# Optimization experiments

Hardware: AMD Instinct MI355X
Metric: run time of the kernel (lower is better)

Reference implementation:

```python
import jax, jax.numpy as jnp
import numpy as np

B, T, TA = 16, 512, 1024
D_REG, D_AUD, HID, HEADS = 512, 512, 256, 4
NREG = 4  # mouth, left_eye, right_eye, nose (dict order)
N = NREG * B * T + B * TA  # total graph nodes


def _build_edges():
    # Faithful, vectorized version of build_graph's edge construction (phoneme_times=None).
    bs = np.arange(B)[:, None]
    ts = np.arange(T)[None, :]
    src, dst = [], []
    # cross-region same-timestep edges, all ordered pairs i != j (edge_attr 0)
    for i in range(NREG):
        for j in range(NREG):
            if i != j:
                n1 = i * B * T + bs * T + ts
                n2 = j * B * T + bs * T + ts
                src.append(n1.ravel()); dst.append(n2.ravel())
    # temporal edges within each region (edge_attr 1)
    tt = np.arange(T - 1)[None, :]
    for i in range(NREG):
        n1 = i * B * T + bs * T + tt
        src.append(n1.ravel()); dst.append((n1 + 1).ravel())
    # eye (region idx 1,2) -> audio alignment edges (edge_attr 3)
    t_aud = (np.arange(T)[None, :] * TA) // T
    audio_start = NREG * B * T
    for i in (1, 2):
        n_eye = i * B * T + bs * T + ts
        n_aud = audio_start + bs * TA + t_aud
        src.append(n_eye.ravel()); dst.append(np.broadcast_to(n_aud, (B, T)).ravel())
    # self loops (PyG GATConv default add_self_loops=True)
    loops = np.arange(N)
    src.append(loops); dst.append(loops)
    return np.concatenate(src).astype(np.int32), np.concatenate(dst).astype(np.int32)


def setup_inputs() -> dict:
    key = jax.random.key(0)
    ks = iter(jax.random.split(key, 48))
    def rn(shape, scale=1.0):
        return jax.random.normal(next(ks), shape, dtype=jnp.float32) * jnp.float32(scale)
    src_np, dst_np = _build_edges()
    inp = {
        'mouth': rn((B, T, D_REG)), 'left_eye': rn((B, T, D_REG)),
        'right_eye': rn((B, T, D_REG)), 'nose': rn((B, T, D_REG)),
        'audio_embeddings': rn((B, TA, D_AUD)),
    }
    s = 1.0 / np.sqrt(D_REG)
    for name in ['mouth', 'left_eye', 'right_eye', 'nose']:
        inp['w_' + name] = rn((D_REG, HID), s)
        inp['b_' + name] = jnp.zeros((HID,), jnp.float32)
    inp['w_audio'] = rn((D_AUD, HID), 1.0 / np.sqrt(D_AUD))
    inp['b_audio'] = jnp.zeros((HID,), jnp.float32)
    # GAT layers: layer 0 in=HID, layers 1,2 in=HID*HEADS; layers 0,1 concat, layer 2 averages heads
    dims_in = [HID, HID * HEADS, HID * HEADS]
    for l, din in enumerate(dims_in):
        concat = l < 2
        inp[f'W{l}'] = rn((din, HEADS * HID), 1.0 / np.sqrt(din))
        inp[f'as{l}'] = rn((HEADS, HID), 0.1)
        inp[f'ad{l}'] = rn((HEADS, HID), 0.1)
        inp[f'bias{l}'] = jnp.zeros((HEADS * HID,) if concat else (HID,), jnp.float32)
    inp['ln_g'] = jnp.ones((HID,), jnp.float32)
    inp['ln_b'] = jnp.zeros((HID,), jnp.float32)
    inp['src'] = jnp.asarray(src_np)
    inp['dst'] = jnp.asarray(dst_np)
    return inp


def _gat(x, W, a_s, a_d, bias, src, dst, concat):
    # PyG GATConv (eval mode): gather -> per-head attention softmax over dst -> scatter-add
    H, C = a_s.shape
    h = (x @ W).reshape(-1, H, C)                      # [N,H,C]
    alpha_s = jnp.sum(h * a_s, -1)                     # [N,H]
    alpha_d = jnp.sum(h * a_d, -1)                     # [N,H]
    e = jax.nn.leaky_relu(alpha_s[src] + alpha_d[dst], 0.2)  # [E,H]
    m = jax.ops.segment_max(e, dst, num_segments=N)
    ex = jnp.exp(e - m[dst])
    denom = jax.ops.segment_sum(ex, dst, num_segments=N)
    alpha = ex / (denom[dst] + jnp.float32(1e-16))
    out = jax.ops.segment_sum(h[src] * alpha[:, :, None], dst, num_segments=N)  # [N,H,C]
    out = out.reshape(-1, H * C) if concat else out.mean(1)
    return out + bias


def _forward(mouth, left_eye, right_eye, nose, audio_embeddings,
             w_mouth, b_mouth, w_left_eye, b_left_eye, w_right_eye, b_right_eye,
             w_nose, b_nose, w_audio, b_audio,
             W0, as0, ad0, bias0, W1, as1, ad1, bias1, W2, as2, ad2, bias2,
             ln_g, ln_b, src, dst):
    x = jnp.concatenate([
        (mouth @ w_mouth + b_mouth).reshape(B * T, HID),
        (left_eye @ w_left_eye + b_left_eye).reshape(B * T, HID),
        (right_eye @ w_right_eye + b_right_eye).reshape(B * T, HID),
        (nose @ w_nose + b_nose).reshape(B * T, HID),
        (audio_embeddings @ w_audio + b_audio).reshape(B * TA, HID),
    ], axis=0)                                          # [N,HID]
    x = _gat(x, W0, as0, ad0, bias0, src, dst, True)    # [N,HID*HEADS]
    x = _gat(x, W1, as1, ad1, bias1, src, dst, True)    # [N,HID*HEADS]
    x = _gat(x, W2, as2, ad2, bias2, src, dst, False)   # [N,HID]
    mu = x.mean(-1, keepdims=True)
    var = jnp.mean(jnp.square(x - mu), -1, keepdims=True)
    x = (x - mu) / jnp.sqrt(var + jnp.float32(1e-5)) * ln_g + ln_b
    nodes_pb = NREG * T + TA
    return x.reshape(B, nodes_pb, HID).mean(1)          # [B,HID]


def reference(mouth, left_eye, right_eye, nose, audio_embeddings,
              w_mouth, b_mouth, w_left_eye, b_left_eye, w_right_eye, b_right_eye,
              w_nose, b_nose, w_audio, b_audio,
              W0, as0, ad0, bias0, W1, as1, ad1, bias1, W2, as2, ad2, bias2,
              ln_g, ln_b, src, dst):
    return _forward(mouth, left_eye, right_eye, nose, audio_embeddings,
                    w_mouth, b_mouth, w_left_eye, b_left_eye, w_right_eye, b_right_eye,
                    w_nose, b_nose, w_audio, b_audio,
                    W0, as0, ad0, bias0, W1, as1, ad1, bias1, W2, as2, ad2, bias2,
                    ln_g, ln_b, src, dst)
```

## Files before the change

kernel.cpp:

```cpp
#include <hip/hip_runtime.h>


typedef unsigned short u16;
typedef unsigned int u32;
typedef __bf16 bf16x8 __attribute__((ext_vector_type(8)));
typedef float f32x4 __attribute__((ext_vector_type(4)));

#define ASYNC16(gp, lp)                                                        \
  __builtin_amdgcn_global_load_lds(                                            \
      (const __attribute__((address_space(1))) void*)(gp),                     \
      (__attribute__((address_space(3))) void*)(lp), 16, 0, 0)

__device__ __forceinline__ u16 f2bf(float f) {
  union { float f; u32 u; } v; v.f = f;
  u32 u = v.u + 0x7FFFu + ((v.u >> 16) & 1u);
  return (u16)(u >> 16);
}
__device__ __forceinline__ float bf2f(u16 x) {
  union { u32 u; float f; } v; v.u = ((u32)x) << 16;
  return v.f;
}
__device__ __forceinline__ float4 load_bf4(const u16* p) {
  ushort4 s = *(const ushort4*)p;
  float4 r; r.x = bf2f(s.x); r.y = bf2f(s.y); r.z = bf2f(s.z); r.w = bf2f(s.w);
  return r;
}
__device__ __forceinline__ float lrelu(float v) { return v > 0.f ? v : 0.2f * v; }
__device__ __forceinline__ float dot4(float4 a, float4 b) {
  return a.x * b.x + a.y * b.y + a.z * b.z + a.w * b.w;
}
__device__ __forceinline__ float wred(float v) {
#pragma unroll
  for (int off = 32; off; off >>= 1) v += __shfl_down(v, off);
  return v;
}
__device__ __forceinline__ float wredx(float v) {
#pragma unroll
  for (int off = 32; off; off >>= 1) v += __shfl_xor(v, off);
  return v;
}

struct PK { const float* W[8]; u16* P[8]; int KB[8]; int NN[8]; int st[9]; };
__global__ __launch_bounds__(256) void pack_kernel(PK p) {
  const int f = blockIdx.x * 4 + (threadIdx.x >> 6);
  const int lane = threadIdx.x & 63;
  int e = 0;
  while (f >= p.st[e + 1]) ++e;
  const int local = f - p.st[e];
  const int KB = p.KB[e], N = p.NN[e];
  const int nt = local / KB, kb = local % KB;
  const float* W = p.W[e] + (size_t)(kb * 32 + (lane >> 4) * 8) * N + nt * 16 + (lane & 15);
  u16* dst = p.P[e] + ((size_t)local * 64 + lane) * 8;
  u16 o[8];
#pragma unroll
  for (int j = 0; j < 8; ++j) o[j] = f2bf(W[(size_t)j * N]);
  *(uint4*)dst = *(uint4*)o;
}

__global__ __launch_bounds__(256) void gemm_kernel(
    const u16* __restrict__ A, const u16* __restrict__ Bp, u16* __restrict__ C,
    int K, int ldc) {
  __shared__ __align__(16) u16 As[2][2][128 * 32];
  const int KB = K >> 5;
  const int KB2 = K >> 6;
  const int w = blockIdx.y * 8 + blockIdx.x;
  const int xcd = w & 7, m = w >> 3;
  const int blockCol = (m & 7) * 128;
  const int blockRow = ((m >> 3) * 8 + xcd) * 128;
  const int tid = threadIdx.x;
  const int wave = tid >> 6, lane = tid & 63;
  const int wr = (wave >> 1) * 64, wc = (wave & 1) * 64;
  const int lr = lane & 15, lq = lane >> 4;
  const int sRow = wave * 16 + (lane >> 2);
  const int sGc = (lane & 3) ^ ((sRow >> 1) & 3);
  const size_t aOff0 = (size_t)(blockRow + sRow) * K + sGc * 8;
  const size_t aOff1 = aOff0 + (size_t)64 * K;
  const int ldsOff0 = wave * 512;
  const int ldsOff1 = 2048 + wave * 512;

  const u16* Bn[4];
#pragma unroll
  for (int ni = 0; ni < 4; ++ni)
    Bn[ni] = Bp + ((size_t)(((blockCol + wc) >> 4) + ni) * KB) * 512 + lane * 8;

  f32x4 acc[4][4] = {};

#pragma unroll
  for (int h = 0; h < 2; ++h) {
    ASYNC16(A + aOff0 + h * 32, As[0][h] + ldsOff0);
    ASYNC16(A + aOff1 + h * 32, As[0][h] + ldsOff1);
  }
  __syncthreads();

  for (int kb2 = 0; kb2 < KB2; ++kb2) {
    const int cb = kb2 & 1;
    if (kb2 + 1 < KB2) {
      const size_t k1 = (size_t)(kb2 + 1) * 64;
#pragma unroll
      for (int h = 0; h < 2; ++h) {
        ASYNC16(A + aOff0 + k1 + h * 32, As[cb ^ 1][h] + ldsOff0);
        ASYNC16(A + aOff1 + k1 + h * 32, As[cb ^ 1][h] + ldsOff1);
      }
    }
#pragma unroll
    for (int h = 0; h < 2; ++h) {
      const int kb = kb2 * 2 + h;
      const u16* cur = As[cb][h];
      bf16x8 bfr[4];
#pragma unroll
      for (int ni = 0; ni < 4; ++ni)
        bfr[ni] = *(const bf16x8*)(Bn[ni] + (size_t)kb * 512);
      bf16x8 af[4];
#pragma unroll
      for (int mi = 0; mi < 4; ++mi) {
        const int R = wr + mi * 16 + lr;
        const int cp = lq ^ ((R >> 1) & 3);
        af[mi] = *(const bf16x8*)(cur + R * 32 + cp * 8);
      }
#pragma unroll
      for (int mi = 0; mi < 4; ++mi)
#pragma unroll
        for (int ni = 0; ni < 4; ++ni)
          acc[mi][ni] = __builtin_amdgcn_mfma_f32_16x16x32_bf16(af[mi], bfr[ni],
                                                                acc[mi][ni], 0, 0, 0);
    }
    __syncthreads();
  }
#pragma unroll
  for (int mi = 0; mi < 4; ++mi)
#pragma unroll
    for (int ni = 0; ni < 4; ++ni) {
      const int col = blockCol + wc + ni * 16 + lr;
#pragma unroll
      for (int r = 0; r < 4; ++r) {
        const int row = blockRow + wr + mi * 16 + lq * 4 + r;
        C[(size_t)row * ldc + col] = f2bf(acc[mi][ni][r]);
      }
    }
}

struct ProjArgs { const float* x[5]; const u16* w[5]; const float* b[5]; };
__global__ __launch_bounds__(256) void proj_kernel(ProjArgs pa,
                                                   u16* __restrict__ C) {
  __shared__ __align__(16) u16 As[128 * 32];
  const int blockRow = blockIdx.y * 128, blockCol = blockIdx.x * 128;
  const int reg = blockRow >= 32768 ? 4 : (blockRow >> 13);
  const int regBase = reg == 4 ? 32768 : reg * 8192;
  const float* Af = pa.x[reg] + (size_t)(blockRow - regBase) * 512;
  const u16* Bp = pa.w[reg];
  const int tid = threadIdx.x;
  const int wave = tid >> 6, lane = tid & 63;
  const int wr = (wave >> 1) * 64, wc = (wave & 1) * 64;
  const int lr = lane & 15, lq = lane >> 4;
  const int rr = tid >> 2;
  const int cphys = tid & 3;
  const int sGc = cphys ^ ((tid >> 3) & 3);

  const u16* Bn[4];
#pragma unroll
  for (int ni = 0; ni < 4; ++ni)
    Bn[ni] = Bp + ((size_t)(((blockCol + wc) >> 4) + ni) * 16) * 512 + lane * 8;

  f32x4 acc[4][4] = {};

  for (int k0 = 0; k0 < 512; k0 += 32) {
    __syncthreads();
    bf16x8 bfr[4];
#pragma unroll
    for (int ni = 0; ni < 4; ++ni)
      bfr[ni] = *(const bf16x8*)(Bn[ni] + (size_t)k0 * 16);
#pragma unroll
    for (int i = 0; i < 2; ++i) {
      const int row = i * 64 + rr;
      const float* ap = Af + (size_t)row * 512 + k0 + sGc * 8;
      float4 f0 = *(const float4*)(ap);
      float4 f1 = *(const float4*)(ap + 4);
      uint4 pk;
      pk.x = (u32)f2bf(f0.x) | ((u32)f2bf(f0.y) << 16);
      pk.y = (u32)f2bf(f0.z) | ((u32)f2bf(f0.w) << 16);
      pk.z = (u32)f2bf(f1.x) | ((u32)f2bf(f1.y) << 16);
      pk.w = (u32)f2bf(f1.z) | ((u32)f2bf(f1.w) << 16);
      *(uint4*)(&As[row * 32 + cphys * 8]) = pk;
    }
    __syncthreads();
    bf16x8 af[4];
#pragma unroll
    for (int mi = 0; mi < 4; ++mi) {
      const int R = wr + mi * 16 + lr;
      const int cp = lq ^ ((R >> 1) & 3);
      af[mi] = *(const bf16x8*)(&As[R * 32 + cp * 8]);
    }
#pragma unroll
    for (int mi = 0; mi < 4; ++mi)
#pragma unroll
      for (int ni = 0; ni < 4; ++ni)
        acc[mi][ni] = __builtin_amdgcn_mfma_f32_16x16x32_bf16(af[mi], bfr[ni],
                                                              acc[mi][ni], 0, 0, 0);
  }
  const float* bias = pa.b[reg];
#pragma unroll
  for (int mi = 0; mi < 4; ++mi)
#pragma unroll
    for (int ni = 0; ni < 4; ++ni) {
      const int col = blockCol + wc + ni * 16 + lr;
      const float bv = bias[col];
#pragma unroll
      for (int r = 0; r < 4; ++r) {
        const int row = blockRow + wr + mi * 16 + lq * 4 + r;
        C[(size_t)row * 256 + col] = f2bf(acc[mi][ni][r] + bv);
      }
    }
}

template <bool MEAN>
__global__ __launch_bounds__(256) void agg_kernel(
    const u16* __restrict__ h, const float* __restrict__ a_s,
    const float* __restrict__ a_d, const float* __restrict__ bias,
    void* __restrict__ out) {
  extern __shared__ float red[];
  const int tid = threadIdx.x;
  const int head = tid >> 6, lane = tid & 63;
  const int c4 = tid * 4;
  const float4 sa = *(const float4*)(a_s + c4);
  const float4 da = *(const float4*)(a_d + c4);
  __shared__ float asL[4][4], adL[4][4], apL[4][4], aeS[4], aeD[4];
  __shared__ float alpha[4][4][5], alphaA[4][3];

  const int bt = blockIdx.x;
  const int b = bt >> 9, t = bt & 511;
  const bool hasPrev = t > 0;
  const int nodeE = 32768 + b * 1024 + 2 * t;
  const int nodeO = nodeE + 1;

  float4 hv[4], hp[4];
#pragma unroll
  for (int r = 0; r < 4; ++r)
    hv[r] = load_bf4(h + (size_t)(r * 8192 + bt) * 1024 + c4);
  float4 hae = load_bf4(h + (size_t)nodeE * 1024 + c4);
  float4 hao = load_bf4(h + (size_t)nodeO * 1024 + c4);
  if (hasPrev) {
#pragma unroll
    for (int r = 0; r < 4; ++r)
      hp[r] = load_bf4(h + (size_t)(r * 8192 + bt - 1) * 1024 + c4);
  }
#pragma unroll
  for (int r = 0; r < 4; ++r) {
    float ss = wred(dot4(hv[r], sa));
    float dd = wred(dot4(hv[r], da));
    float sp = hasPrev ? wred(dot4(hp[r], sa)) : 0.f;
    if (lane == 0) { asL[r][head] = ss; adL[r][head] = dd; apL[r][head] = sp; }
  }
  {
    float se = wred(dot4(hae, sa));
    float de = wred(dot4(hae, da));
    if (lane == 0) { aeS[head] = se; aeD[head] = de; }
  }
  __syncthreads();
  if (tid < 16) {
    const int j = tid >> 2, hh = tid & 3;
    const float ad = adL[j][hh];
    float e[5];
#pragma unroll
    for (int r = 0; r < 4; ++r) e[r] = lrelu(asL[r][hh] + ad);
    int cnt = 4;
    if (hasPrev) { e[4] = lrelu(apL[j][hh] + ad); cnt = 5; }
    float mx = e[0];
    for (int k = 1; k < cnt; ++k) mx = fmaxf(mx, e[k]);
    float s = 0.f, ex[5];
    for (int k = 0; k < cnt; ++k) { ex[k] = __expf(e[k] - mx); s += ex[k]; }
    const float inv = 1.f / (s + 1e-16f);
#pragma unroll
    for (int k = 0; k < 5; ++k) alpha[j][hh][k] = (k < cnt) ? ex[k] * inv : 0.f;
  } else if (tid < 20) {
    const int hh = tid - 16;
    const float ad = aeD[hh];
    const float e0 = lrelu(aeS[hh] + ad);
    const float e1 = lrelu(asL[1][hh] + ad);
    const float e2 = lrelu(asL[2][hh] + ad);
    const float mx = fmaxf(e0, fmaxf(e1, e2));
    const float x0 = __expf(e0 - mx), x1 = __expf(e1 - mx), x2 = __expf(e2 - mx);
    const float inv = 1.f / (x0 + x1 + x2 + 1e-16f);
    alphaA[hh][0] = x0 * inv; alphaA[hh][1] = x1 * inv; alphaA[hh][2] = x2 * inv;
  }
  __syncthreads();

  float4 av[6];
#pragma unroll
  for (int j = 0; j < 4; ++j) {
    const float* al = &alpha[j][head][0];
    float4 acc;
    acc.x = al[0] * hv[0].x + al[1] * hv[1].x + al[2] * hv[2].x + al[3] * hv[3].x;
    acc.y = al[0] * hv[0].y + al[1] * hv[1].y + al[2] * hv[2].y + al[3] * hv[3].y;
    acc.z = al[0] * hv[0].z + al[1] * hv[1].z + al[2] * hv[2].z + al[3] * hv[3].z;
    acc.w = al[0] * hv[0].w + al[1] * hv[1].w + al[2] * hv[2].w + al[3] * hv[3].w;
    if (hasPrev) {
      const float a4 = al[4];
      acc.x += a4 * hp[j].x; acc.y += a4 * hp[j].y;
      acc.z += a4 * hp[j].z; acc.w += a4 * hp[j].w;
    }
    av[j] = acc;
  }
  {
    const float a0 = alphaA[head][0], a1 = alphaA[head][1], a2 = alphaA[head][2];
    float4 acc;
    acc.x = a0 * hae.x + a1 * hv[1].x + a2 * hv[2].x;
    acc.y = a0 * hae.y + a1 * hv[1].y + a2 * hv[2].y;
    acc.z = a0 * hae.z + a1 * hv[1].z + a2 * hv[2].z;
    acc.w = a0 * hae.w + a1 * hv[1].w + a2 * hv[2].w;
    av[4] = acc;
    av[5] = hao;
  }

  if constexpr (!MEAN) {
    const float4 bv = *(const float4*)(bias + c4);
    u16* ob = (u16*)out;
    size_t rows[6];
#pragma unroll
    for (int j = 0; j < 4; ++j) rows[j] = (size_t)(j * 8192 + bt);
    rows[4] = (size_t)nodeE; rows[5] = (size_t)nodeO;
#pragma unroll
    for (int k = 0; k < 6; ++k) {
      ushort4 o;
      o.x = f2bf(av[k].x + bv.x); o.y = f2bf(av[k].y + bv.y);
      o.z = f2bf(av[k].z + bv.z); o.w = f2bf(av[k].w + bv.w);
      *(ushort4*)(ob + rows[k] * 1024 + c4) = o;
    }
  } else {
#pragma unroll
    for (int k = 0; k < 6; ++k) *(float4*)(&red[k * 1024 + c4]) = av[k];
    __syncthreads();
    const float bb = bias[tid];
    float* of = (float*)out;
    size_t rows[6];
#pragma unroll
    for (int j = 0; j < 4; ++j) rows[j] = (size_t)(j * 8192 + bt);
    rows[4] = (size_t)nodeE; rows[5] = (size_t)nodeO;
#pragma unroll
    for (int k = 0; k < 6; ++k) {
      const float v = 0.25f * (red[k * 1024 + tid] + red[k * 1024 + tid + 256] +
                               red[k * 1024 + tid + 512] + red[k * 1024 + tid + 768]) + bb;
      of[rows[k] * 256 + tid] = v;
    }
  }
}

__global__ __launch_bounds__(256) void ln_pool_kernel(
    const float* __restrict__ xf, const float* __restrict__ g,
    const float* __restrict__ bb, float* __restrict__ part) {
  const int tid = threadIdx.x;
  const int wave = tid >> 6, lane = tid & 63;
  const int node0 = blockIdx.x * 64 + wave * 16;
  const float4 g4 = *(const float4*)(g + lane * 4);
  const float4 b4 = *(const float4*)(bb + lane * 4);
  float4 acc = {0.f, 0.f, 0.f, 0.f};
  for (int i = 0; i < 16; ++i) {
    const float4 v = *(const float4*)(xf + (size_t)(node0 + i) * 256 + lane * 4);
    const float s = wredx(v.x + v.y + v.z + v.w);
    const float q = wredx(v.x * v.x + v.y * v.y + v.z * v.z + v.w * v.w);
    const float mean = s * (1.f / 256.f);
    const float var = q * (1.f / 256.f) - mean * mean;
    const float rstd = rsqrtf(var + 1e-5f);
    acc.x += (v.x - mean) * rstd * g4.x + b4.x;
    acc.y += (v.y - mean) * rstd * g4.y + b4.y;
    acc.z += (v.z - mean) * rstd * g4.z + b4.z;
    acc.w += (v.w - mean) * rstd * g4.w + b4.w;
  }
  *(float4*)(part + (size_t)(blockIdx.x * 4 + wave) * 256 + lane * 4) = acc;
}

__global__ __launch_bounds__(256) void pool2_kernel(const float* __restrict__ part,
                                                    float* __restrict__ out) {
  const int chunk = blockIdx.x;
  const int c = threadIdx.x;
  float s = 0.f;
  for (int i = 0; i < 192; ++i) s += part[(size_t)(chunk * 192 + i) * 256 + c];
  out[chunk * 256 + c] = s * (1.f / 3072.f);
}

extern "C" void kernel_launch(void* const* d_in, const int* in_sizes, int n_in,
                              void* d_out, int out_size, void* d_ws, size_t ws_size,
                              hipStream_t stream) {
  const float* x_reg[4] = {(const float*)d_in[0], (const float*)d_in[1],
                           (const float*)d_in[2], (const float*)d_in[3]};
  const float* audio = (const float*)d_in[4];
  const float* w_reg[4] = {(const float*)d_in[5], (const float*)d_in[7],
                           (const float*)d_in[9], (const float*)d_in[11]};
  const float* b_reg[4] = {(const float*)d_in[6], (const float*)d_in[8],
                           (const float*)d_in[10], (const float*)d_in[12]};
  const float* w_aud = (const float*)d_in[13];
  const float* b_aud = (const float*)d_in[14];
  const float* Wl[3] = {(const float*)d_in[15], (const float*)d_in[19],
                        (const float*)d_in[23]};
  const float* as_in[3] = {(const float*)d_in[16], (const float*)d_in[20],
                           (const float*)d_in[24]};
  const float* ad_in[3] = {(const float*)d_in[17], (const float*)d_in[21],
                           (const float*)d_in[25]};
  const float* bias_l[3] = {(const float*)d_in[18], (const float*)d_in[22],
                            (const float*)d_in[26]};
  const float* ln_g = (const float*)d_in[27];
  const float* ln_b = (const float*)d_in[28];

  char* ws = (char*)d_ws;
  u16* h_bf = (u16*)ws;
  float* part = (float*)ws;
  u16* xb = (u16*)(ws + 100663296);
  float* xf = (float*)xb;
  u16* wt = (u16*)(ws + 201326592);

  u16* wtp[5];
  for (int r = 0; r < 5; ++r) wtp[r] = wt + (size_t)r * 131072;
  u16* wt0 = wt + 655360;
  u16* wt1 = wt + 917504;
  u16* wt2 = wt + 1966080;

  PK pk;
  for (int r = 0; r < 4; ++r) { pk.W[r] = w_reg[r]; pk.P[r] = wtp[r]; pk.KB[r] = 16; pk.NN[r] = 256; }
  pk.W[4] = w_aud; pk.P[4] = wtp[4]; pk.KB[4] = 16; pk.NN[4] = 256;
  pk.W[5] = Wl[0]; pk.P[5] = wt0; pk.KB[5] = 8;  pk.NN[5] = 1024;
  pk.W[6] = Wl[1]; pk.P[6] = wt1; pk.KB[6] = 32; pk.NN[6] = 1024;
  pk.W[7] = Wl[2]; pk.P[7] = wt2; pk.KB[7] = 32; pk.NN[7] = 1024;
  pk.st[0] = 0;
  {
    const int nfr[8] = {256, 256, 256, 256, 256, 512, 2048, 2048};
    int acc = 0;
    for (int e = 0; e < 8; ++e) { acc += nfr[e]; pk.st[e + 1] = acc; }
  }
  pack_kernel<<<pk.st[8] / 4, 256, 0, stream>>>(pk);

  ProjArgs pa;
  for (int r = 0; r < 4; ++r) { pa.x[r] = x_reg[r]; pa.w[r] = wtp[r]; pa.b[r] = b_reg[r]; }
  pa.x[4] = audio; pa.w[4] = wtp[4]; pa.b[4] = b_aud;
  proj_kernel<<<dim3(2, 384), 256, 0, stream>>>(pa, xb);

  const u16* wl[3] = {wt0, wt1, wt2};
  const int Kl[3] = {256, 1024, 1024};
  const size_t dynLds = 6 * 1024 * sizeof(float);
  for (int l = 0; l < 3; ++l) {
    gemm_kernel<<<dim3(8, 384), 256, 0, stream>>>(xb, wl[l], h_bf, Kl[l], 1024);
    if (l < 2)
      agg_kernel<false><<<8192, 256, 0, stream>>>(h_bf, as_in[l], ad_in[l],
                                                  bias_l[l], xb);
    else
      agg_kernel<true><<<8192, 256, dynLds, stream>>>(h_bf, as_in[l], ad_in[l],
                                                      bias_l[l], xf);
  }

  ln_pool_kernel<<<768, 256, 0, stream>>>(xf, ln_g, ln_b, part);
  pool2_kernel<<<16, 256, 0, stream>>>(part, (float*)d_out);
}
```

Before: 616.9 us.

## Fold input projection into GAT layer-0 weights and drop agg shared-memory syncs

Precomputes combined weights W_region·W0 and biases b_region·W0 on device, so one K=512 GEMM per region writes layer-0 features directly. This removes the separate projection GEMM and its intermediate write/read. The layer-0/1 aggregation now computes attention with xor-shuffle reductions in every lane instead of LDS plus two barriers. The GEMM also hoists both B-fragment loads ahead of the async A prefetch. Folding the weights raises the layer-0 GEMM from K=256 to K=512 and adds several small setup kernels plus an extra bf16 rounding of the combined weights.

Result: slower. 690.7 us (+12.0%).

```diff
diff --git a/kernel.cpp b/kernel.cpp
--- a/kernel.cpp
+++ b/kernel.cpp
@@ -40,7 +40,7 @@
   return v;
 }
 
-struct PK { const float* W[8]; u16* P[8]; int KB[8]; int NN[8]; int st[9]; };
+struct PK { const float* W[3]; u16* P[3]; int KB[3]; int NN[3]; int st[4]; };
 __global__ __launch_bounds__(256) void pack_kernel(PK p) {
   const int f = blockIdx.x * 4 + (threadIdx.x >> 6);
   const int lane = threadIdx.x & 63;
@@ -55,6 +55,41 @@
 #pragma unroll
   for (int j = 0; j < 8; ++j) o[j] = f2bf(W[(size_t)j * N]);
   *(uint4*)dst = *(uint4*)o;
+}
+
+struct CW { const float* w[5]; };
+__global__ __launch_bounds__(256) void cvtw_kernel(CW a, u16* __restrict__ dst) {
+  const int i = blockIdx.x * 256 + threadIdx.x;
+  const float* src = a.w[i >> 15];
+  float4 v = ((const float4*)src)[i & 32767];
+  ushort4 o;
+  o.x = f2bf(v.x); o.y = f2bf(v.y); o.z = f2bf(v.z); o.w = f2bf(v.w);
+  ((ushort4*)dst)[i] = o;
+}
+
+struct BC { const float* br[5]; };
+__global__ __launch_bounds__(256) void bc_kernel(BC a, const float* __restrict__ W0,
+                                                 float* __restrict__ bc) {
+  const int r = blockIdx.x >> 2;
+  const int n = (blockIdx.x & 3) * 256 + threadIdx.x;
+  const float* b = a.br[r];
+  float acc = 0.f;
+  for (int k = 0; k < 256; ++k) acc += b[k] * W0[(size_t)k * 1024 + n];
+  bc[r * 1024 + n] = acc;
+}
+
+__global__ __launch_bounds__(256) void packwc_kernel(const u16* __restrict__ Wrm,
+                                                     u16* __restrict__ P) {
+  const int f = blockIdx.x * 4 + (threadIdx.x >> 6);
+  const int lane = threadIdx.x & 63;
+  const int region = f >> 10, local = f & 1023;
+  const int nt = local >> 4, kb = local & 15;
+  const u16* W = Wrm + (size_t)(region * 512 + kb * 32 + (lane >> 4) * 8) * 1024 +
+                 nt * 16 + (lane & 15);
+  u16 o[8];
+#pragma unroll
+  for (int j = 0; j < 8; ++j) o[j] = W[(size_t)j * 1024];
+  *(uint4*)(P + ((size_t)f * 64 + lane) * 8) = *(uint4*)o;
 }
 
 __global__ __launch_bounds__(256) void gemm_kernel(
@@ -94,6 +129,12 @@
 
   for (int kb2 = 0; kb2 < KB2; ++kb2) {
     const int cb = kb2 & 1;
+    bf16x8 bfr[2][4];
+#pragma unroll
+    for (int h = 0; h < 2; ++h)
+#pragma unroll
+      for (int ni = 0; ni < 4; ++ni)
+        bfr[h][ni] = *(const bf16x8*)(Bn[ni] + (size_t)(kb2 * 2 + h) * 512);
     if (kb2 + 1 < KB2) {
       const size_t k1 = (size_t)(kb2 + 1) * 64;
 #pragma unroll
@@ -104,12 +145,7 @@
     }
 #pragma unroll
     for (int h = 0; h < 2; ++h) {
-      const int kb = kb2 * 2 + h;
       const u16* cur = As[cb][h];
-      bf16x8 bfr[4];
-#pragma unroll
-      for (int ni = 0; ni < 4; ++ni)
-        bfr[ni] = *(const bf16x8*)(Bn[ni] + (size_t)kb * 512);
       bf16x8 af[4];
 #pragma unroll
       for (int mi = 0; mi < 4; ++mi) {
@@ -121,7 +157,7 @@
       for (int mi = 0; mi < 4; ++mi)
 #pragma unroll
         for (int ni = 0; ni < 4; ++ni)
-          acc[mi][ni] = __builtin_amdgcn_mfma_f32_16x16x32_bf16(af[mi], bfr[ni],
+          acc[mi][ni] = __builtin_amdgcn_mfma_f32_16x16x32_bf16(af[mi], bfr[h][ni],
                                                                 acc[mi][ni], 0, 0, 0);
     }
     __syncthreads();
@@ -139,15 +175,20 @@
     }
 }
 
-struct ProjArgs { const float* x[5]; const u16* w[5]; const float* b[5]; };
-__global__ __launch_bounds__(256) void proj_kernel(ProjArgs pa,
-                                                   u16* __restrict__ C) {
+struct P0Args { const float* x[5]; };
+__global__ __launch_bounds__(256) void projL0_kernel(P0Args pa,
+                                                     const u16* __restrict__ Bp0,
+                                                     const float* __restrict__ bc,
+                                                     u16* __restrict__ C) {
   __shared__ __align__(16) u16 As[128 * 32];
-  const int blockRow = blockIdx.y * 128, blockCol = blockIdx.x * 128;
+  const int w = blockIdx.y * 8 + blockIdx.x;
+  const int xcd = w & 7, m = w >> 3;
+  const int blockCol = (m & 7) * 128;
+  const int blockRow = ((m >> 3) * 8 + xcd) * 128;
   const int reg = blockRow >= 32768 ? 4 : (blockRow >> 13);
   const int regBase = reg == 4 ? 32768 : reg * 8192;
   const float* Af = pa.x[reg] + (size_t)(blockRow - regBase) * 512;
-  const u16* Bp = pa.w[reg];
+  const u16* Bp = Bp0 + (size_t)reg * 524288;
   const int tid = threadIdx.x;
   const int wave = tid >> 6, lane = tid & 63;
   const int wr = (wave >> 1) * 64, wc = (wave & 1) * 64;
@@ -197,7 +238,7 @@
         acc[mi][ni] = __builtin_amdgcn_mfma_f32_16x16x32_bf16(af[mi], bfr[ni],
                                                               acc[mi][ni], 0, 0, 0);
   }
-  const float* bias = pa.b[reg];
+  const float* bias = bc + reg * 1024;
 #pragma unroll
   for (int mi = 0; mi < 4; ++mi)
 #pragma unroll
@@ -207,7 +248,7 @@
 #pragma unroll
       for (int r = 0; r < 4; ++r) {
         const int row = blockRow + wr + mi * 16 + lq * 4 + r;
-        C[(size_t)row * 256 + col] = f2bf(acc[mi][ni][r] + bv);
+        C[(size_t)row * 1024 + col] = f2bf(acc[mi][ni][r] + bv);
       }
     }
 }
@@ -223,8 +264,6 @@
   const int c4 = tid * 4;
   const float4 sa = *(const float4*)(a_s + c4);
   const float4 da = *(const float4*)(a_d + c4);
-  __shared__ float asL[4][4], adL[4][4], apL[4][4], aeS[4], aeD[4];
-  __shared__ float alpha[4][4][5], alphaA[4][3];
 
   const int bt = blockIdx.x;
   const int b = bt >> 9, t = bt & 511;
@@ -243,89 +282,142 @@
     for (int r = 0; r < 4; ++r)
       hp[r] = load_bf4(h + (size_t)(r * 8192 + bt - 1) * 1024 + c4);
   }
-#pragma unroll
-  for (int r = 0; r < 4; ++r) {
-    float ss = wred(dot4(hv[r], sa));
-    float dd = wred(dot4(hv[r], da));
-    float sp = hasPrev ? wred(dot4(hp[r], sa)) : 0.f;
-    if (lane == 0) { asL[r][head] = ss; adL[r][head] = dd; apL[r][head] = sp; }
-  }
-  {
-    float se = wred(dot4(hae, sa));
-    float de = wred(dot4(hae, da));
-    if (lane == 0) { aeS[head] = se; aeD[head] = de; }
-  }
-  __syncthreads();
-  if (tid < 16) {
-    const int j = tid >> 2, hh = tid & 3;
-    const float ad = adL[j][hh];
-    float e[5];
-#pragma unroll
-    for (int r = 0; r < 4; ++r) e[r] = lrelu(asL[r][hh] + ad);
-    int cnt = 4;
-    if (hasPrev) { e[4] = lrelu(apL[j][hh] + ad); cnt = 5; }
-    float mx = e[0];
-    for (int k = 1; k < cnt; ++k) mx = fmaxf(mx, e[k]);
-    float s = 0.f, ex[5];
-    for (int k = 0; k < cnt; ++k) { ex[k] = __expf(e[k] - mx); s += ex[k]; }
-    const float inv = 1.f / (s + 1e-16f);
-#pragma unroll
-    for (int k = 0; k < 5; ++k) alpha[j][hh][k] = (k < cnt) ? ex[k] * inv : 0.f;
-  } else if (tid < 20) {
-    const int hh = tid - 16;
-    const float ad = aeD[hh];
-    const float e0 = lrelu(aeS[hh] + ad);
-    const float e1 = lrelu(asL[1][hh] + ad);
-    const float e2 = lrelu(asL[2][hh] + ad);
-    const float mx = fmaxf(e0, fmaxf(e1, e2));
-    const float x0 = __expf(e0 - mx), x1 = __expf(e1 - mx), x2 = __expf(e2 - mx);
-    const float inv = 1.f / (x0 + x1 + x2 + 1e-16f);
-    alphaA[hh][0] = x0 * inv; alphaA[hh][1] = x1 * inv; alphaA[hh][2] = x2 * inv;
-  }
-  __syncthreads();
-
-  float4 av[6];
-#pragma unroll
-  for (int j = 0; j < 4; ++j) {
-    const float* al = &alpha[j][head][0];
-    float4 acc;
-    acc.x = al[0] * hv[0].x + al[1] * hv[1].x + al[2] * hv[2].x + al[3] * hv[3].x;
-    acc.y = al[0] * hv[0].y + al[1] * hv[1].y + al[2] * hv[2].y + al[3] * hv[3].y;
-    acc.z = al[0] * hv[0].z + al[1] * hv[1].z + al[2] * hv[2].z + al[3] * hv[3].z;
-    acc.w = al[0] * hv[0].w + al[1] * hv[1].w + al[2] * hv[2].w + al[3] * hv[3].w;
+
+  if constexpr (!MEAN) {
+    float ss[4], dd[4], sp[4];
+#pragma unroll
+    for (int r = 0; r < 4; ++r) {
+      ss[r] = wredx(dot4(hv[r], sa));
+      dd[r] = wredx(dot4(hv[r], da));
+    }
     if (hasPrev) {
-      const float a4 = al[4];
-      acc.x += a4 * hp[j].x; acc.y += a4 * hp[j].y;
-      acc.z += a4 * hp[j].z; acc.w += a4 * hp[j].w;
-    }
-    av[j] = acc;
-  }
-  {
-    const float a0 = alphaA[head][0], a1 = alphaA[head][1], a2 = alphaA[head][2];
-    float4 acc;
-    acc.x = a0 * hae.x + a1 * hv[1].x + a2 * hv[2].x;
-    acc.y = a0 * hae.y + a1 * hv[1].y + a2 * hv[2].y;
-    acc.z = a0 * hae.z + a1 * hv[1].z + a2 * hv[2].z;
-    acc.w = a0 * hae.w + a1 * hv[1].w + a2 * hv[2].w;
-    av[4] = acc;
-    av[5] = hao;
-  }
-
-  if constexpr (!MEAN) {
+#pragma unroll
+      for (int r = 0; r < 4; ++r) sp[r] = wredx(dot4(hp[r], sa));
+    }
+    const float se = wredx(dot4(hae, sa));
+    const float de = wredx(dot4(hae, da));
+
     const float4 bv = *(const float4*)(bias + c4);
     u16* ob = (u16*)out;
-    size_t rows[6];
-#pragma unroll
-    for (int j = 0; j < 4; ++j) rows[j] = (size_t)(j * 8192 + bt);
-    rows[4] = (size_t)nodeE; rows[5] = (size_t)nodeO;
-#pragma unroll
-    for (int k = 0; k < 6; ++k) {
+#pragma unroll
+    for (int j = 0; j < 4; ++j) {
+      const float ad = dd[j];
+      float e0 = lrelu(ss[0] + ad), e1 = lrelu(ss[1] + ad);
+      float e2 = lrelu(ss[2] + ad), e3 = lrelu(ss[3] + ad);
+      float mx = fmaxf(fmaxf(e0, e1), fmaxf(e2, e3));
+      float e4 = 0.f;
+      if (hasPrev) { e4 = lrelu(sp[j] + ad); mx = fmaxf(mx, e4); }
+      const float x0 = __expf(e0 - mx), x1 = __expf(e1 - mx);
+      const float x2 = __expf(e2 - mx), x3 = __expf(e3 - mx);
+      const float x4 = hasPrev ? __expf(e4 - mx) : 0.f;
+      const float inv = 1.f / (x0 + x1 + x2 + x3 + x4 + 1e-16f);
+      const float a0 = x0 * inv, a1 = x1 * inv, a2 = x2 * inv, a3 = x3 * inv;
+      const float a4 = x4 * inv;
+      float4 acc;
+      acc.x = a0 * hv[0].x + a1 * hv[1].x + a2 * hv[2].x + a3 * hv[3].x;
+      acc.y = a0 * hv[0].y + a1 * hv[1].y + a2 * hv[2].y + a3 * hv[3].y;
+      acc.z = a0 * hv[0].z + a1 * hv[1].z + a2 * hv[2].z + a3 * hv[3].z;
+      acc.w = a0 * hv[0].w + a1 * hv[1].w + a2 * hv[2].w + a3 * hv[3].w;
+      if (hasPrev) {
+        acc.x += a4 * hp[j].x; acc.y += a4 * hp[j].y;
+        acc.z += a4 * hp[j].z; acc.w += a4 * hp[j].w;
+      }
       ushort4 o;
-      o.x = f2bf(av[k].x + bv.x); o.y = f2bf(av[k].y + bv.y);
-      o.z = f2bf(av[k].z + bv.z); o.w = f2bf(av[k].w + bv.w);
-      *(ushort4*)(ob + rows[k] * 1024 + c4) = o;
+      o.x = f2bf(acc.x + bv.x); o.y = f2bf(acc.y + bv.y);
+      o.z = f2bf(acc.z + bv.z); o.w = f2bf(acc.w + bv.w);
+      *(ushort4*)(ob + (size_t)(j * 8192 + bt) * 1024 + c4) = o;
+    }
+    {
+      const float e0 = lrelu(se + de);
+      const float e1 = lrelu(ss[1] + de);
+      const float e2 = lrelu(ss[2] + de);
+      const float mx = fmaxf(e0, fmaxf(e1, e2));
+      const float x0 = __expf(e0 - mx), x1 = __expf(e1 - mx), x2 = __expf(e2 - mx);
+      const float inv = 1.f / (x0 + x1 + x2 + 1e-16f);
+      const float a0 = x0 * inv, a1 = x1 * inv, a2 = x2 * inv;
+      float4 acc;
+      acc.x = a0 * hae.x + a1 * hv[1].x + a2 * hv[2].x;
+      acc.y = a0 * hae.y + a1 * hv[1].y + a2 * hv[2].y;
+      acc.z = a0 * hae.z + a1 * hv[1].z + a2 * hv[2].z;
+      acc.w = a0 * hae.w + a1 * hv[1].w + a2 * hv[2].w;
+      ushort4 oe, oo;
+      oe.x = f2bf(acc.x + bv.x); oe.y = f2bf(acc.y + bv.y);
+      oe.z = f2bf(acc.z + bv.z); oe.w = f2bf(acc.w + bv.w);
+      oo.x = f2bf(hao.x + bv.x); oo.y = f2bf(hao.y + bv.y);
+      oo.z = f2bf(hao.z + bv.z); oo.w = f2bf(hao.w + bv.w);
+      *(ushort4*)(ob + (size_t)nodeE * 1024 + c4) = oe;
+      *(ushort4*)(ob + (size_t)nodeO * 1024 + c4) = oo;
     }
   } else {
+    __shared__ float asL[4][4], adL[4][4], apL[4][4], aeS[4], aeD[4];
+    __shared__ float alpha[4][4][5], alphaA[4][3];
+#pragma unroll
+    for (int r = 0; r < 4; ++r) {
+      float ss = wred(dot4(hv[r], sa));
+      float dd = wred(dot4(hv[r], da));
+      float sp = hasPrev ? wred(dot4(hp[r], sa)) : 0.f;
+      if (lane == 0) { asL[r][head] = ss; adL[r][head] = dd; apL[r][head] = sp; }
+    }
+    {
+      float sev = wred(dot4(hae, sa));
+      float dev = wred(dot4(hae, da));
+      if (lane == 0) { aeS[head] = sev; aeD[head] = dev; }
+    }
+    __syncthreads();
+    if (tid < 16) {
+      const int j = tid >> 2, hh = tid & 3;
+      const float ad = adL[j][hh];
+      float e[5];
+#pragma unroll
+      for (int r = 0; r < 4; ++r) e[r] = lrelu(asL[r][hh] + ad);
+      int cnt = 4;
+      if (hasPrev) { e[4] = lrelu(apL[j][hh] + ad); cnt = 5; }
+      float mx = e[0];
+      for (int k = 1; k < cnt; ++k) mx = fmaxf(mx, e[k]);
+      float s = 0.f, ex[5];
+      for (int k = 0; k < cnt; ++k) { ex[k] = __expf(e[k] - mx); s += ex[k]; }
+      const float inv = 1.f / (s + 1e-16f);
+#pragma unroll
+      for (int k = 0; k < 5; ++k) alpha[j][hh][k] = (k < cnt) ? ex[k] * inv : 0.f;
+    } else if (tid < 20) {
+      const int hh = tid - 16;
+      const float ad = aeD[hh];
+      const float e0 = lrelu(aeS[hh] + ad);
+      const float e1 = lrelu(asL[1][hh] + ad);
+      const float e2 = lrelu(asL[2][hh] + ad);
+      const float mx = fmaxf(e0, fmaxf(e1, e2));
+      const float x0 = __expf(e0 - mx), x1 = __expf(e1 - mx), x2 = __expf(e2 - mx);
+      const float inv = 1.f / (x0 + x1 + x2 + 1e-16f);
+      alphaA[hh][0] = x0 * inv; alphaA[hh][1] = x1 * inv; alphaA[hh][2] = x2 * inv;
+    }
+    __syncthreads();
+
+    float4 av[6];
+#pragma unroll
+    for (int j = 0; j < 4; ++j) {
+      const float* al = &alpha[j][head][0];
+      float4 acc;
+      acc.x = al[0] * hv[0].x + al[1] * hv[1].x + al[2] * hv[2].x + al[3] * hv[3].x;
+      acc.y = al[0] * hv[0].y + al[1] * hv[1].y + al[2] * hv[2].y + al[3] * hv[3].y;
+      acc.z = al[0] * hv[0].z + al[1] * hv[1].z + al[2] * hv[2].z + al[3] * hv[3].z;
+      acc.w = al[0] * hv[0].w + al[1] * hv[1].w + al[2] * hv[2].w + al[3] * hv[3].w;
+      if (hasPrev) {
+        const float a4 = al[4];
+        acc.x += a4 * hp[j].x; acc.y += a4 * hp[j].y;
+        acc.z += a4 * hp[j].z; acc.w += a4 * hp[j].w;
+      }
+      av[j] = acc;
+    }
+    {
+      const float a0 = alphaA[head][0], a1 = alphaA[head][1], a2 = alphaA[head][2];
+      float4 acc;
+      acc.x = a0 * hae.x + a1 * hv[1].x + a2 * hv[2].x;
+      acc.y = a0 * hae.y + a1 * hv[1].y + a2 * hv[2].y;
+      acc.z = a0 * hae.z + a1 * hv[1].z + a2 * hv[2].z;
+      acc.w = a0 * hae.w + a1 * hv[1].w + a2 * hv[2].w;
+      av[4] = acc;
+      av[5] = hao;
+    }
 #pragma unroll
     for (int k = 0; k < 6; ++k) *(float4*)(&red[k * 1024 + c4]) = av[k];
     __syncthreads();
@@ -402,48 +494,49 @@
 
   char* ws = (char*)d_ws;
   u16* h_bf = (u16*)ws;
+  u16* wr_bf = (u16*)ws;
+  u16* wc_rm = (u16*)(ws + 2097152);
   float* part = (float*)ws;
   u16* xb = (u16*)(ws + 100663296);
+  u16* wcp = xb;
   float* xf = (float*)xb;
-  u16* wt = (u16*)(ws + 201326592);
-
-  u16* wtp[5];
-  for (int r = 0; r < 5; ++r) wtp[r] = wt + (size_t)r * 131072;
-  u16* wt0 = wt + 655360;
-  u16* wt1 = wt + 917504;
-  u16* wt2 = wt + 1966080;
+  u16* wt0 = (u16*)(ws + 201326592);
+  u16* wt1 = wt0 + 262144;
+  u16* wt2 = wt1 + 1048576;
+  float* bc = (float*)(ws + 201326592 + 4718592);
 
   PK pk;
-  for (int r = 0; r < 4; ++r) { pk.W[r] = w_reg[r]; pk.P[r] = wtp[r]; pk.KB[r] = 16; pk.NN[r] = 256; }
-  pk.W[4] = w_aud; pk.P[4] = wtp[4]; pk.KB[4] = 16; pk.NN[4] = 256;
-  pk.W[5] = Wl[0]; pk.P[5] = wt0; pk.KB[5] = 8;  pk.NN[5] = 1024;
-  pk.W[6] = Wl[1]; pk.P[6] = wt1; pk.KB[6] = 32; pk.NN[6] = 1024;
-  pk.W[7] = Wl[2]; pk.P[7] = wt2; pk.KB[7] = 32; pk.NN[7] = 1024;
-  pk.st[0] = 0;
-  {
-    const int nfr[8] = {256, 256, 256, 256, 256, 512, 2048, 2048};
-    int acc = 0;
-    for (int e = 0; e < 8; ++e) { acc += nfr[e]; pk.st[e + 1] = acc; }
-  }
-  pack_kernel<<<pk.st[8] / 4, 256, 0, stream>>>(pk);
-
-  ProjArgs pa;
-  for (int r = 0; r < 4; ++r) { pa.x[r] = x_reg[r]; pa.w[r] = wtp[r]; pa.b[r] = b_reg[r]; }
-  pa.x[4] = audio; pa.w[4] = wtp[4]; pa.b[4] = b_aud;
-  proj_kernel<<<dim3(2, 384), 256, 0, stream>>>(pa, xb);
-
-  const u16* wl[3] = {wt0, wt1, wt2};
-  const int Kl[3] = {256, 1024, 1024};
+  pk.W[0] = Wl[0]; pk.P[0] = wt0; pk.KB[0] = 8;  pk.NN[0] = 1024;
+  pk.W[1] = Wl[1]; pk.P[1] = wt1; pk.KB[1] = 32; pk.NN[1] = 1024;
+  pk.W[2] = Wl[2]; pk.P[2] = wt2; pk.KB[2] = 32; pk.NN[2] = 1024;
+  pk.st[0] = 0; pk.st[1] = 512; pk.st[2] = 2560; pk.st[3] = 4608;
+  pack_kernel<<<1152, 256, 0, stream>>>(pk);
+
+  CW cw;
+  for (int r = 0; r < 4; ++r) cw.w[r] = w_reg[r];
+  cw.w[4] = w_aud;
+  cvtw_kernel<<<640, 256, 0, stream>>>(cw, wr_bf);
+  gemm_kernel<<<dim3(8, 24), 256, 0, stream>>>(wr_bf, wt0, wc_rm, 256, 1024);
+  BC bca;
+  for (int r = 0; r < 4; ++r) bca.br[r] = b_reg[r];
+  bca.br[4] = b_aud;
+  bc_kernel<<<20, 256, 0, stream>>>(bca, Wl[0], bc);
+  packwc_kernel<<<1280, 256, 0, stream>>>(wc_rm, wcp);
+
+  P0Args pa;
+  for (int r = 0; r < 4; ++r) pa.x[r] = x_reg[r];
+  pa.x[4] = audio;
+  projL0_kernel<<<dim3(8, 384), 256, 0, stream>>>(pa, wcp, bc, h_bf);
+
   const size_t dynLds = 6 * 1024 * sizeof(float);
-  for (int l = 0; l < 3; ++l) {
-    gemm_kernel<<<dim3(8, 384), 256, 0, stream>>>(xb, wl[l], h_bf, Kl[l], 1024);
-    if (l < 2)
-      agg_kernel<false><<<8192, 256, 0, stream>>>(h_bf, as_in[l], ad_in[l],
-                                                  bias_l[l], xb);
-    else
-      agg_kernel<true><<<8192, 256, dynLds, stream>>>(h_bf, as_in[l], ad_in[l],
-                                                      bias_l[l], xf);
-  }
+  agg_kernel<false><<<8192, 256, 0, stream>>>(h_bf, as_in[0], ad_in[0],
+                                              bias_l[0], xb);
+  gemm_kernel<<<dim3(8, 384), 256, 0, stream>>>(xb, wt1, h_bf, 1024, 1024);
+  agg_kernel<false><<<8192, 256, 0, stream>>>(h_bf, as_in[1], ad_in[1],
+                                              bias_l[1], xb);
+  gemm_kernel<<<dim3(8, 384), 256, 0, stream>>>(xb, wt2, h_bf, 1024, 1024);
+  agg_kernel<true><<<8192, 256, dynLds, stream>>>(h_bf, as_in[2], ad_in[2],
+                                                  bias_l[2], xf);
 
   ln_pool_kernel<<<768, 256, 0, stream>>>(xf, ln_g, ln_b, part);
   pool2_kernel<<<16, 256, 0, stream>>>(part, (float*)d_out);
```
